# Kernel optimization log

Measured on AMD Instinct MI355X. Metric: run time of the kernel, lower is better.

Reference implementation:

```python
import jax, jax.numpy as jnp
import numpy as np

N = 20000      # nodes
E = 320000     # edges
F_IN = 64      # input_dim
HID = 128      # hidden_dim
H = 2          # heads (hard-coded in BGA)
G = 64         # num graphs (batch_step_dim[0])
MID = 32       # middle_dim
OUT = 1        # output_dim
EPS = 1e-5


def setup_inputs() -> dict:
    key = jax.random.key(0)
    ks = jax.random.split(key, 24)
    p = lambda k, shape: jax.random.normal(k, shape, jnp.float32) * 0.05
    inp = {}
    inp["x"] = jax.random.normal(ks[0], (N, F_IN), jnp.float32)
    inp["edge_index"] = jax.random.randint(ks[1], (2, E), 0, N)
    inp["atten_edge_index"] = jax.random.randint(ks[2], (2, E), 0, N)
    inp["batch_index"] = jnp.sort(jax.random.randint(ks[3], (N,), 0, G))
    # GANConv 0 MLP (2-layer: Linear->BN->ReLU->Linear)
    inp["g0_w1"] = p(ks[4], (F_IN, HID)); inp["g0_b1"] = jnp.zeros((HID,), jnp.float32)
    inp["g0_bn_g"] = jnp.ones((HID,), jnp.float32); inp["g0_bn_b"] = jnp.zeros((HID,), jnp.float32)
    inp["g0_w2"] = p(ks[5], (HID, HID)); inp["g0_b2"] = jnp.zeros((HID,), jnp.float32)
    # GANConv 1 MLP
    inp["g1_w1"] = p(ks[6], (HID, HID)); inp["g1_b1"] = jnp.zeros((HID,), jnp.float32)
    inp["g1_bn_g"] = jnp.ones((HID,), jnp.float32); inp["g1_bn_b"] = jnp.zeros((HID,), jnp.float32)
    inp["g1_w2"] = p(ks[7], (HID, HID)); inp["g1_b2"] = jnp.zeros((HID,), jnp.float32)
    # BGA batch norms after each GANConv
    inp["bn0_g"] = jnp.ones((HID,), jnp.float32); inp["bn0_b"] = jnp.zeros((HID,), jnp.float32)
    inp["bn1_g"] = jnp.ones((HID,), jnp.float32); inp["bn1_b"] = jnp.zeros((HID,), jnp.float32)
    # ATTConv atten_self: in=HID, out=HID, heads=2, concat=True
    inp["a1_wl"] = p(ks[8], (HID, H * HID)); inp["a1_bl"] = jnp.zeros((H * HID,), jnp.float32)
    inp["a1_wr"] = p(ks[9], (HID, H * HID)); inp["a1_br"] = jnp.zeros((H * HID,), jnp.float32)
    inp["a1_att"] = p(ks[10], (H, HID))
    inp["a1_bias"] = jnp.zeros((H * HID,), jnp.float32)
    # ATTConv atten: in=H*HID, out=HID, heads=2, concat=False (mean over heads)
    inp["a2_wl"] = p(ks[11], (H * HID, H * HID)); inp["a2_bl"] = jnp.zeros((H * HID,), jnp.float32)
    inp["a2_wr"] = p(ks[12], (H * HID, H * HID)); inp["a2_br"] = jnp.zeros((H * HID,), jnp.float32)
    inp["a2_att"] = p(ks[13], (H, HID))
    inp["a2_bias"] = jnp.zeros((HID,), jnp.float32)
    # prediction heads (only layer 0 and last are used)
    inp["pred0_w"] = p(ks[14], (F_IN, MID)); inp["pred0_b"] = jnp.zeros((MID,), jnp.float32)
    inp["predL_w"] = p(ks[15], (HID, MID)); inp["predL_b"] = jnp.zeros((MID,), jnp.float32)
    inp["out_w"] = p(ks[16], (MID, OUT)); inp["out_b"] = jnp.zeros((OUT,), jnp.float32)
    return inp


def _bn(x, g, b):  # training-mode batch norm over node axis
    m = x.mean(0)
    v = x.var(0)
    return (x - m) * jax.lax.rsqrt(v + EPS) * g + b


def _mlp2(x, w1, b1, bn_g, bn_b, w2, b2):
    h = jax.nn.relu(_bn(x @ w1 + b1, bn_g, bn_b))
    return h @ w2 + b2


def _gan_conv(x, edge_index, w1, b1, bn_g, bn_b, w2, b2):
    row, col = edge_index[0], edge_index[1]
    agg = jax.ops.segment_sum(x[col], row, num_segments=x.shape[0])
    return _mlp2(x + agg, w1, b1, bn_g, bn_b, w2, b2)


def _att_conv(x, edge_index, wl, bl, wr, br, att, bias, concat):
    # GATv2-style: e = leaky_relu(x_i + x_j); alpha = softmax_dst(<e, att>)
    n = x.shape[0]
    xl = (x @ wl + bl).reshape(n, H, HID)  # source proj
    xr = (x @ wr + br).reshape(n, H, HID)  # target proj
    src, dst = edge_index[0], edge_index[1]
    e = jax.nn.leaky_relu(xl[src] + xr[dst], 0.2)          # [E,H,C]
    logit = jnp.einsum('ehc,hc->eh', e, att)               # [E,H]
    lmax = jax.ops.segment_max(logit, dst, num_segments=n)
    w = jnp.exp(logit - lmax[dst])
    denom = jax.ops.segment_sum(w, dst, num_segments=n)
    alpha = w / (denom[dst] + 1e-16)                       # [E,H]
    out = jax.ops.segment_sum(xl[src] * alpha[:, :, None], dst, num_segments=n)
    if concat:
        out = out.reshape(n, H * HID)
    else:
        out = out.mean(1)
    return out + bias, alpha


def reference(x, edge_index, atten_edge_index, batch_index,
              g0_w1, g0_b1, g0_bn_g, g0_bn_b, g0_w2, g0_b2,
              g1_w1, g1_b1, g1_bn_g, g1_bn_b, g1_w2, g1_b2,
              bn0_g, bn0_b, bn1_g, bn1_b,
              a1_wl, a1_bl, a1_wr, a1_br, a1_att, a1_bias,
              a2_wl, a2_bl, a2_wr, a2_br, a2_att, a2_bias,
              pred0_w, pred0_b, predL_w, predL_b, out_w, out_b):
    h0 = x
    h1 = jax.nn.relu(_bn(_gan_conv(h0, edge_index, g0_w1, g0_b1, g0_bn_g, g0_bn_b, g0_w2, g0_b2), bn0_g, bn0_b))
    h2 = jax.nn.relu(_bn(_gan_conv(h1, edge_index, g1_w1, g1_b1, g1_bn_g, g1_bn_b, g1_w2, g1_b2), bn1_g, bn1_b))
    emb, _ = _att_conv(h2, edge_index, a1_wl, a1_bl, a1_wr, a1_br, a1_att, a1_bias, concat=True)
    emb = jax.nn.relu(emb)
    atten_out, alpha = _att_conv(emb, atten_edge_index, a2_wl, a2_bl, a2_wr, a2_br, a2_att, a2_bias, concat=False)
    atten_out = jax.nn.relu(atten_out)
    pool0 = jax.ops.segment_sum(h0, batch_index, num_segments=G)
    poolL = jax.ops.segment_sum(atten_out, batch_index, num_segments=G)
    out_h = jax.nn.relu((pool0 @ pred0_w + pred0_b) + (poolL @ predL_w + predL_b))
    outputs = out_h @ out_w + out_b
    return (outputs, atten_out, alpha)
```

## Files before the change

kernel.cpp:

```cpp
#include <hip/hip_runtime.h>
#include <hip/hip_bf16.h>

#define N_NODES 20000
#define E_EDGES 320000
#define F_INN   64
#define HID     128
#define HEADS   2
#define HC      (HEADS * HID)
#define G_GR    64
#define MIDD    32
#define EPSV    1e-5f
#define NBUK    79

#define CDIV(a, b) (((a) + (b) - 1) / (b))

typedef __attribute__((ext_vector_type(8))) short          bf16x8;
typedef __attribute__((ext_vector_type(4))) float          f32x4;
typedef __attribute__((ext_vector_type(8))) unsigned short u16x8;

__device__ inline float bf2f(unsigned short u) { return __uint_as_float((unsigned)u << 16); }
__device__ inline unsigned short f2bf(float f) {
    unsigned u = __float_as_uint(f);
    unsigned r = u + 0x7FFFu + ((u >> 16) & 1u);
    return (unsigned short)(r >> 16);
}

struct Csr3 {
    const int* key[3];
    const int* other[3];
    int* deg;
    int* rowptr[3];
    int* out[3];
    int2* tmp;
    int* bcur;
};

__global__ void k_hist3(Csr3 c) {
    int e = blockIdx.x * blockDim.x + threadIdx.x;
    int y = blockIdx.y;
    if (e < E_EDGES) atomicAdd(&c.deg[y * N_NODES + c.key[y][e]], 1);
}

__global__ __launch_bounds__(1024) void k_scan3(Csr3 c) {
    const int PER = (N_NODES + 1023) / 1024;
    __shared__ int part[1024];
    const int y = blockIdx.x;
    const int* deg = c.deg + y * N_NODES;
    int* rowptr = c.rowptr[y];
    const int tid = threadIdx.x;
    const int base = tid * PER;
    int lv[PER];
    int lsum = 0;
#pragma unroll
    for (int i = 0; i < PER; i++) {
        int idx = base + i;
        int v = (idx < N_NODES) ? deg[idx] : 0;
        lv[i] = v; lsum += v;
    }
    part[tid] = lsum;
    __syncthreads();
    for (int off = 1; off < 1024; off <<= 1) {
        int t = (tid >= off) ? part[tid - off] : 0;
        __syncthreads();
        part[tid] += t;
        __syncthreads();
    }
    int run = part[tid] - lsum;
    if (tid == 0) rowptr[0] = 0;
#pragma unroll
    for (int i = 0; i < PER; i++) {
        int idx = base + i;
        if (idx < N_NODES) {
            run += lv[i];
            rowptr[idx + 1] = run;
        }
        if (idx < N_NODES && i == 0) rowptr[idx] = part[tid] - lsum;
    }
    __syncthreads();
    if (tid < NBUK) c.bcur[y * NBUK + tid] = rowptr[tid << 8];
}

__global__ __launch_bounds__(256) void k_bucketA(Csr3 c) {
    __shared__ int hist[NBUK], base[NBUK], off[NBUK];
    const int y = blockIdx.y;
    const int chunk0 = blockIdx.x * 4096;
    const int t = threadIdx.x;
    for (int i = t; i < NBUK; i += 256) { hist[i] = 0; off[i] = 0; }
    __syncthreads();
    int keys[16], vals[16], bks[16];
#pragma unroll
    for (int i = 0; i < 16; i++) {
        int e = chunk0 + (i << 8) + t;
        bool ok = (e < E_EDGES);
        int k = ok ? c.key[y][e] : 0;
        keys[i] = k;
        vals[i] = ok ? ((y == 2) ? e : c.other[y][e]) : 0;
        bks[i] = ok ? (k >> 8) : -1;
        if (ok) atomicAdd(&hist[k >> 8], 1);
    }
    __syncthreads();
    if (t < NBUK && hist[t] > 0) base[t] = atomicAdd(&c.bcur[y * NBUK + t], hist[t]);
    __syncthreads();
    int2* ty = c.tmp + (size_t)y * E_EDGES;
#pragma unroll
    for (int i = 0; i < 16; i++) {
        int b = bks[i];
        if (b >= 0) {
            int o = atomicAdd(&off[b], 1);
            ty[base[b] + o] = make_int2(keys[i], vals[i]);
        }
    }
}

__global__ __launch_bounds__(256) void k_bucketB(Csr3 c) {
    __shared__ int cnt[256], lbase[256], run[256];
    const int y = blockIdx.y;
    const int b = blockIdx.x;
    const int nbase = b << 8;
    const int t = threadIdx.x;
    cnt[t] = 0; run[t] = 0;
    __syncthreads();
    const int* rowptr = c.rowptr[y];
    const int start = rowptr[nbase];
    const int nend = min(nbase + 256, N_NODES);
    const int end = rowptr[nend];
    const int2* ty = c.tmp + (size_t)y * E_EDGES;
    for (int i = start + t; i < end; i += 256)
        atomicAdd(&cnt[ty[i].x - nbase], 1);
    __syncthreads();
    int v = cnt[t];
    lbase[t] = v;
    __syncthreads();
    for (int off = 1; off < 256; off <<= 1) {
        int u = (t >= off) ? lbase[t - off] : 0;
        __syncthreads();
        lbase[t] += u;
        __syncthreads();
    }
    int excl = lbase[t] - v;
    __syncthreads();
    lbase[t] = excl;
    __syncthreads();
    int* outy = c.out[y];
    for (int i = start + t; i < end; i += 256) {
        int2 kv = ty[i];
        int k = kv.x - nbase;
        int o = atomicAdd(&run[k], 1);
        outy[start + lbase[k] + o] = kv.y;
    }
}

__global__ __launch_bounds__(256) void k_gather_f32(const float4* __restrict__ x,
                                                    const int* __restrict__ rowptr,
                                                    const int* __restrict__ srcs,
                                                    unsigned short* __restrict__ z) {
    int gid = blockIdx.x * blockDim.x + threadIdx.x;
    int n = gid >> 4;
    if (n >= N_NODES) return;
    int q = gid & 15;
    float4 acc = x[((size_t)n << 4) + q];
    int p1 = rowptr[n + 1];
    for (int p = rowptr[n]; p < p1; p++) {
        float4 v = x[((size_t)srcs[p] << 4) + q];
        acc.x += v.x; acc.y += v.y; acc.z += v.z; acc.w += v.w;
    }
    ushort4 o;
    o.x = f2bf(acc.x); o.y = f2bf(acc.y); o.z = f2bf(acc.z); o.w = f2bf(acc.w);
    *(ushort4*)&z[((size_t)n << 6) + (q << 2)] = o;
}

__global__ __launch_bounds__(256) void k_gather_bn(const u16x8* __restrict__ raw,
                                                   const int* __restrict__ rowptr,
                                                   const int* __restrict__ srcs,
                                                   const float* __restrict__ bn_sums,
                                                   const float* __restrict__ g,
                                                   const float* __restrict__ b,
                                                   u16x8* __restrict__ z) {
    int gid = blockIdx.x * blockDim.x + threadIdx.x;
    int n = gid >> 4;
    if (n >= N_NODES) return;
    int q = gid & 15;
    float sc[8], sh[8];
#pragma unroll
    for (int i = 0; i < 8; i++) {
        int c = (q << 3) + i;
        float mean = bn_sums[c] / N_NODES;
        float istd = rsqrtf(bn_sums[HID + c] / N_NODES - mean * mean + EPSV);
        float s = istd * g[c];
        sc[i] = s;
        sh[i] = b[c] - mean * s;
    }
    u16x8 u0 = raw[((size_t)n << 4) + q];
    float acc[8];
#pragma unroll
    for (int i = 0; i < 8; i++) acc[i] = fmaxf(bf2f(u0[i]) * sc[i] + sh[i], 0.f);
    int p1 = rowptr[n + 1];
    for (int p = rowptr[n]; p < p1; p++) {
        u16x8 v = raw[((size_t)srcs[p] << 4) + q];
#pragma unroll
        for (int i = 0; i < 8; i++) acc[i] += fmaxf(bf2f(v[i]) * sc[i] + sh[i], 0.f);
    }
    u16x8 o;
#pragma unroll
    for (int i = 0; i < 8; i++) o[i] = f2bf(acc[i]);
    z[((size_t)n << 4) + q] = o;
}

struct WtJob  { const float* src; unsigned short* dst; int K; int N; };
struct WtJobs { WtJob j[8]; };
__global__ void k_wt_cast(WtJobs jobs) {
    WtJob jb = jobs.j[blockIdx.y];
    int total = jb.K * jb.N;
    for (int i = blockIdx.x * blockDim.x + threadIdx.x; i < total; i += gridDim.x * blockDim.x) {
        int nn = i / jb.K, kk = i - nn * jb.K;
        jb.dst[i] = f2bf(jb.src[(size_t)kk * jb.N + nn]);
    }
}

template <int STATS, int BNA, int TM, int BIAS2>
__global__ __launch_bounds__(256) void k_mfma_gemm(const unsigned short* __restrict__ A,
                                                   const unsigned short* __restrict__ Wt,
                                                   const float* __restrict__ biasL,
                                                   const float* __restrict__ biasR,
                                                   unsigned short* __restrict__ Cout,
                                                   int M, int K, int N,
                                                   float* __restrict__ stats_sums,
                                                   const float* __restrict__ bn_sums,
                                                   const float* __restrict__ bn_g,
                                                   const float* __restrict__ bn_b) {
    constexpr int BNF = (TM == 128) ? 4 : 2;
    __shared__ unsigned short As[TM][40];
    __shared__ unsigned short Bs[128][40];
    __shared__ float s_scale[BNA ? HID : 1], s_shift[BNA ? HID : 1];
    const int t = threadIdx.x;
    if (BNA) {
        if (t < HID) {
            float mean = bn_sums[t] / M;
            float istd = rsqrtf(bn_sums[HID + t] / M - mean * mean + EPSV);
            float s = istd * bn_g[t];
            s_scale[t] = s;
            s_shift[t] = bn_b[t] - mean * s;
        }
        __syncthreads();
    }
    const int wave = t >> 6, lane = t & 63;
    const int row0 = blockIdx.y * TM, col0 = blockIdx.x * 128;
    const int wm = (TM == 128) ? ((wave & 1) << 6) : 0;
    const int wn = (TM == 128) ? ((wave >> 1) << 6) : (wave << 5);
    const int lm = lane & 15, lk = (lane >> 4) << 3;
    constexpr int APASS = TM / 64;
    f32x4 acc[4][BNF] = {};
    for (int k0 = 0; k0 < K; k0 += 32) {
        u16x8 av[APASS], wv[2];
#pragma unroll
        for (int i = 0; i < APASS; i++) {
            int c = t + (i << 8);
            int r = c >> 2, ko = (c & 3) << 3;
            u16x8 zv = {};
            int gr = row0 + r;
            av[i] = (gr < M) ? *(const u16x8*)&A[(size_t)gr * K + k0 + ko] : zv;
            if (BNA) {
#pragma unroll
                for (int j = 0; j < 8; j++) {
                    int kc = k0 + ko + j;
                    float v = fmaxf(bf2f(av[i][j]) * s_scale[kc] + s_shift[kc], 0.f);
                    av[i][j] = f2bf(v);
                }
            }
        }
#pragma unroll
        for (int i = 0; i < 2; i++) {
            int c = t + (i << 8);
            int r = c >> 2, ko = (c & 3) << 3;
            wv[i] = *(const u16x8*)&Wt[(size_t)(col0 + r) * K + k0 + ko];
        }
        __syncthreads();
#pragma unroll
        for (int i = 0; i < APASS; i++) {
            int c = t + (i << 8);
            int r = c >> 2, ko = (c & 3) << 3;
            *(u16x8*)&As[r][ko] = av[i];
        }
#pragma unroll
        for (int i = 0; i < 2; i++) {
            int c = t + (i << 8);
            int r = c >> 2, ko = (c & 3) << 3;
            *(u16x8*)&Bs[r][ko] = wv[i];
        }
        __syncthreads();
        bf16x8 af[4], bfm[BNF];
#pragma unroll
        for (int i = 0; i < 4; i++) af[i]  = *(const bf16x8*)&As[wm + (i << 4) + lm][lk];
#pragma unroll
        for (int j = 0; j < BNF; j++) bfm[j] = *(const bf16x8*)&Bs[wn + (j << 4) + lm][lk];
#pragma unroll
        for (int i = 0; i < 4; i++)
#pragma unroll
            for (int j = 0; j < BNF; j++)
                acc[i][j] = __builtin_amdgcn_mfma_f32_16x16x32_bf16(af[i], bfm[j], acc[i][j], 0, 0, 0);
    }
    const int lr4 = (lane >> 4) << 2;
    float s1[BNF], s2[BNF];
#pragma unroll
    for (int j = 0; j < BNF; j++) { s1[j] = 0.f; s2[j] = 0.f; }
#pragma unroll
    for (int j = 0; j < BNF; j++) {
        int col = col0 + wn + (j << 4) + lm;
        float bv = BIAS2 ? ((col < 256) ? biasL[col] : biasR[col - 256]) : biasL[col];
#pragma unroll
        for (int i = 0; i < 4; i++) {
#pragma unroll
            for (int r = 0; r < 4; r++) {
                int row = row0 + wm + (i << 4) + lr4 + r;
                if (row < M) {
                    float v = acc[i][j][r] + bv;
                    Cout[(size_t)row * N + col] = f2bf(v);
                    if (STATS) { s1[j] += v; s2[j] += v * v; }
                }
            }
        }
    }
    if (STATS) {
#pragma unroll
        for (int j = 0; j < BNF; j++) {
            s1[j] += __shfl_xor(s1[j], 16, 64); s1[j] += __shfl_xor(s1[j], 32, 64);
            s2[j] += __shfl_xor(s2[j], 16, 64); s2[j] += __shfl_xor(s2[j], 32, 64);
        }
        if ((lane >> 4) == 0) {
#pragma unroll
            for (int j = 0; j < BNF; j++) {
                int col = col0 + wn + (j << 4) + lm;
                atomicAdd(&stats_sums[col], s1[j]);
                atomicAdd(&stats_sums[HID + col], s2[j]);
            }
        }
    }
}

#define ATT_CAP 192
template <int CONCAT, int WITH_ALPHA>
__global__ __launch_bounds__(256) void k_att_fused(const ushort4* __restrict__ Q,
                                                   const int* __restrict__ rowptr,
                                                   const int* __restrict__ plist,
                                                   const int* __restrict__ other,
                                                   const float* __restrict__ att,
                                                   const float* __restrict__ bias,
                                                   void* __restrict__ outp,
                                                   float* __restrict__ alpha_out) {
    __shared__ float s_lg[4][ATT_CAP][2];
    const int t = threadIdx.x;
    const int wave = t >> 6, l = t & 63;
    const int n = blockIdx.x * 4 + wave;
    const int h = l >> 5;
    ushort4 ur = Q[((size_t)n << 7) + 64 + l];
    float xr4[4] = {bf2f(ur.x), bf2f(ur.y), bf2f(ur.z), bf2f(ur.w)};
    const float* ap = &att[h * HID + ((l & 31) << 2)];
    float at4[4] = {ap[0], ap[1], ap[2], ap[3]};
    const int p0 = rowptr[n], p1 = rowptr[n + 1];

    float m = -INFINITY, ssum = 0.f;
    float acc[4] = {0.f, 0.f, 0.f, 0.f};

#define ATT_SRC(p) (WITH_ALPHA ? other[plist[p]] : plist[p])

#define ATT_LOGIT(uv, x4, tl) do { \
        x4[0] = bf2f(uv.x); x4[1] = bf2f(uv.y); x4[2] = bf2f(uv.z); x4[3] = bf2f(uv.w); \
        float v0 = x4[0] + xr4[0]; v0 = (v0 > 0.f) ? v0 : 0.2f * v0; \
        float v1 = x4[1] + xr4[1]; v1 = (v1 > 0.f) ? v1 : 0.2f * v1; \
        float v2 = x4[2] + xr4[2]; v2 = (v2 > 0.f) ? v2 : 0.2f * v2; \
        float v3 = x4[3] + xr4[3]; v3 = (v3 > 0.f) ? v3 : 0.2f * v3; \
        tl = at4[0] * v0 + at4[1] * v1 + at4[2] * v2 + at4[3] * v3; \
    } while (0)

#define ATT_ONLINE(x4, tl, idx) do { \
        float mn = fmaxf(m, tl); \
        float sc = __expf(m - mn); \
        float w  = __expf(tl - mn); \
        ssum = ssum * sc + w; \
        acc[0] = acc[0] * sc + w * x4[0]; \
        acc[1] = acc[1] * sc + w * x4[1]; \
        acc[2] = acc[2] * sc + w * x4[2]; \
        acc[3] = acc[3] * sc + w * x4[3]; \
        m = mn; \
        if (WITH_ALPHA && (idx) < ATT_CAP && (l & 31) == 0) s_lg[wave][idx][h] = tl; \
    } while (0)

    int p = p0;
    for (; p + 4 <= p1; p += 4) {
        float x4[4][4], tl[4];
        ushort4 uv[4];
        int ss[4];
#pragma unroll
        for (int j = 0; j < 4; j++) ss[j] = ATT_SRC(p + j);
#pragma unroll
        for (int j = 0; j < 4; j++) uv[j] = Q[((size_t)ss[j] << 7) + l];
#pragma unroll
        for (int j = 0; j < 4; j++) ATT_LOGIT(uv[j], x4[j], tl[j]);
#pragma unroll
        for (int k = 1; k <= 16; k <<= 1) {
#pragma unroll
            for (int j = 0; j < 4; j++) tl[j] += __shfl_xor(tl[j], k, 64);
        }
#pragma unroll
        for (int j = 0; j < 4; j++) ATT_ONLINE(x4[j], tl[j], p + j - p0);
    }
    for (; p < p1; p++) {
        float x4[4], tl;
        ushort4 uv = Q[((size_t)ATT_SRC(p) << 7) + l];
        ATT_LOGIT(uv, x4, tl);
#pragma unroll
        for (int k = 1; k <= 16; k <<= 1) tl += __shfl_xor(tl, k, 64);
        ATT_ONLINE(x4, tl, p - p0);
    }
    float inv = 1.f / (ssum + 1e-16f);

    if (WITH_ALPHA) {
        float m_o   = __shfl_xor(m, 32, 64);
        float inv_o = __shfl_xor(inv, 32, 64);
        float m2[2], i2[2];
        m2[h] = m; m2[1 - h] = m_o;
        i2[h] = inv; i2[1 - h] = inv_o;
        int cnt = p1 - p0;
        int ccnt = (cnt < ATT_CAP) ? cnt : ATT_CAP;
        for (int i = l; i < ccnt * 2; i += 64) {
            int idx = i >> 1, hh = i & 1;
            float a = __expf(s_lg[wave][idx][hh] - m2[hh]) * i2[hh];
            alpha_out[plist[p0 + idx] * HEADS + hh] = a;
        }
        for (int pp = p0 + ATT_CAP; pp < p1; pp++) {
            float x4[4], tl;
            ushort4 uv = Q[((size_t)ATT_SRC(pp) << 7) + l];
            ATT_LOGIT(uv, x4, tl);
#pragma unroll
            for (int k = 1; k <= 16; k <<= 1) tl += __shfl_xor(tl, k, 64);
            if ((l & 31) == 0) alpha_out[plist[pp] * HEADS + h] = __expf(tl - m) * inv;
        }
    }

    if (CONCAT) {
        const float* bp = &bias[l << 2];
        ushort4 o;
        o.x = f2bf(fmaxf(acc[0] * inv + bp[0], 0.f));
        o.y = f2bf(fmaxf(acc[1] * inv + bp[1], 0.f));
        o.z = f2bf(fmaxf(acc[2] * inv + bp[2], 0.f));
        o.w = f2bf(fmaxf(acc[3] * inv + bp[3], 0.f));
        ((ushort4*)outp)[((size_t)n << 6) + l] = o;
    } else {
        float o[4];
#pragma unroll
        for (int i = 0; i < 4; i++) {
            float v = acc[i] * inv;
            float other_v = __shfl_xor(v, 32, 64);
            o[i] = 0.5f * (v + other_v);
        }
        if (l < 32) {
            const float* bp = &bias[(l & 31) << 2];
            float4 ov;
            ov.x = fmaxf(o[0] + bp[0], 0.f); ov.y = fmaxf(o[1] + bp[1], 0.f);
            ov.z = fmaxf(o[2] + bp[2], 0.f); ov.w = fmaxf(o[3] + bp[3], 0.f);
            ((float4*)outp)[((size_t)n << 5) + l] = ov;
        }
    }
#undef ATT_SRC
#undef ATT_LOGIT
#undef ATT_ONLINE
}

template <int C>
__global__ __launch_bounds__(256) void k_pool_atomic(const float* __restrict__ X,
                                                     const int* __restrict__ batch,
                                                     float* __restrict__ pool, int npb) {
    const int RP = 256 / C;
    int c = threadIdx.x & (C - 1);
    int rofs = threadIdx.x / C;
    int i0 = blockIdx.x * npb;
    int i1 = min(i0 + npb, N_NODES);
    float acc = 0.f;
    int gcur = -1;
    for (int i = i0 + rofs; i < i1; i += RP) {
        int g = batch[i];
        if (g != gcur) {
            if (gcur >= 0) atomicAdd(&pool[gcur * C + c], acc);
            acc = 0.f; gcur = g;
        }
        acc += X[(size_t)i * C + c];
    }
    if (gcur >= 0) atomicAdd(&pool[gcur * C + c], acc);
}

__global__ void k_head(const float* __restrict__ pool0, const float* __restrict__ poolL,
                       const float* __restrict__ p0w, const float* __restrict__ p0b,
                       const float* __restrict__ pLw, const float* __restrict__ pLb,
                       const float* __restrict__ ow, const float* __restrict__ ob,
                       float* __restrict__ outputs) {
    int g = blockIdx.x;
    int m = threadIdx.x;
    __shared__ float sh[MIDD];
    if (m < MIDD) {
        float s = p0b[m] + pLb[m];
        for (int k = 0; k < F_INN; k++) s += pool0[g * F_INN + k] * p0w[k * MIDD + m];
        for (int k = 0; k < HID; k++)  s += poolL[g * HID + k] * pLw[k * MIDD + m];
        sh[m] = fmaxf(s, 0.f);
    }
    __syncthreads();
    if (m == 0) {
        float s = ob[0];
        for (int k = 0; k < MIDD; k++) s += sh[k] * ow[k];
        outputs[g] = s;
    }
}

extern "C" void kernel_launch(void* const* d_in, const int* in_sizes, int n_in,
                              void* d_out, int out_size, void* d_ws, size_t ws_size,
                              hipStream_t stream) {
    const float* x      = (const float*)d_in[0];
    const int*   ei     = (const int*)d_in[1];
    const int*   aei    = (const int*)d_in[2];
    const int*   batch  = (const int*)d_in[3];
    const float* g0_w1  = (const float*)d_in[4];
    const float* g0_b1  = (const float*)d_in[5];
    const float* g0_bng = (const float*)d_in[6];
    const float* g0_bnb = (const float*)d_in[7];
    const float* g0_w2  = (const float*)d_in[8];
    const float* g0_b2  = (const float*)d_in[9];
    const float* g1_w1  = (const float*)d_in[10];
    const float* g1_b1  = (const float*)d_in[11];
    const float* g1_bng = (const float*)d_in[12];
    const float* g1_bnb = (const float*)d_in[13];
    const float* g1_w2  = (const float*)d_in[14];
    const float* g1_b2  = (const float*)d_in[15];
    const float* bn0_g  = (const float*)d_in[16];
    const float* bn0_b  = (const float*)d_in[17];
    const float* bn1_g  = (const float*)d_in[18];
    const float* bn1_b  = (const float*)d_in[19];
    const float* a1_wl  = (const float*)d_in[20];
    const float* a1_bl  = (const float*)d_in[21];
    const float* a1_wr  = (const float*)d_in[22];
    const float* a1_br  = (const float*)d_in[23];
    const float* a1_att = (const float*)d_in[24];
    const float* a1_bias= (const float*)d_in[25];
    const float* a2_wl  = (const float*)d_in[26];
    const float* a2_bl  = (const float*)d_in[27];
    const float* a2_wr  = (const float*)d_in[28];
    const float* a2_br  = (const float*)d_in[29];
    const float* a2_att = (const float*)d_in[30];
    const float* a2_bias= (const float*)d_in[31];
    const float* p0w    = (const float*)d_in[32];
    const float* p0b    = (const float*)d_in[33];
    const float* pLw    = (const float*)d_in[34];
    const float* pLb    = (const float*)d_in[35];
    const float* ow     = (const float*)d_in[36];
    const float* ob     = (const float*)d_in[37];

    float* out_head  = (float*)d_out;
    float* atten_out = out_head + G_GR;
    float* alpha_out = atten_out + (size_t)N_NODES * HID;

    float* ws = (float*)d_ws;
    float* sums4 = ws;
    float* pool0 = sums4 + 4 * 256;
    float* poolL = pool0 + G_GR * F_INN;
    int*   deg3  = (int*)(poolL + G_GR * HID);
    const size_t zero_bytes = (4 * 256 + G_GR * F_INN + G_GR * HID + 3 * N_NODES) * 4;

    int* ip = deg3 + 3 * N_NODES;
    int* bcur = ip; ip += 3 * NBUK;
    int* rowptr[3]; int* payload[3];
    for (int c = 0; c < 3; c++) {
        rowptr[c]  = ip; ip += N_NODES + 1;
        payload[c] = ip; ip += E_EDGES;
    }
    int2* tmp3 = (int2*)ip; ip += 2 * 3 * E_EDGES;
    const size_t NB = (size_t)N_NODES * HC;
    unsigned short* B1 = (unsigned short*)ip;
    unsigned short* B2 = B1 + NB;
    unsigned short* Qb = B2 + NB;
    unsigned short* g0w1t = Qb + 2 * NB;
    unsigned short* g0w2t = g0w1t + 128 * 64;
    unsigned short* g1w1t = g0w2t + 128 * 128;
    unsigned short* g1w2t = g1w1t + 128 * 128;
    unsigned short* a1wlt = g1w2t + 128 * 128;
    unsigned short* a1wrt = a1wlt + 256 * 128;
    unsigned short* a2wlt = a1wrt + 256 * 128;
    unsigned short* a2wrt = a2wlt + 256 * 256;

    const int* e_row = ei;
    const int* e_col = ei + E_EDGES;
    const int* a_src = aei;
    const int* a_dst = aei + E_EDGES;

    const int TB = 256;
#define GRID1(n) dim3(CDIV((n), TB))

    {
        WtJobs jobs;
        jobs.j[0] = {g0_w1, g0w1t, F_INN, HID};
        jobs.j[1] = {g0_w2, g0w2t, HID,   HID};
        jobs.j[2] = {g1_w1, g1w1t, HID,   HID};
        jobs.j[3] = {g1_w2, g1w2t, HID,   HID};
        jobs.j[4] = {a1_wl, a1wlt, HID,   HC};
        jobs.j[5] = {a1_wr, a1wrt, HID,   HC};
        jobs.j[6] = {a2_wl, a2wlt, HC,    HC};
        jobs.j[7] = {a2_wr, a2wrt, HC,    HC};
        k_wt_cast<<<dim3(32, 8), TB, 0, stream>>>(jobs);
    }

    hipMemsetAsync(sums4, 0, zero_bytes, stream);
    {
        Csr3 c;
        c.key[0] = e_row; c.other[0] = e_col;
        c.key[1] = e_col; c.other[1] = e_row;
        c.key[2] = a_dst; c.other[2] = a_src;
        c.deg = deg3; c.tmp = tmp3; c.bcur = bcur;
        for (int i = 0; i < 3; i++) { c.rowptr[i] = rowptr[i]; c.out[i] = payload[i]; }
        k_hist3<<<dim3(CDIV(E_EDGES, TB), 3), TB, 0, stream>>>(c);
        k_scan3<<<dim3(3), 1024, 0, stream>>>(c);
        k_bucketA<<<dim3(CDIV(E_EDGES, 4096), 3), TB, 0, stream>>>(c);
        k_bucketB<<<dim3(NBUK, 3), TB, 0, stream>>>(c);
    }

    const dim3 gemm_g1(1, CDIV(N_NODES, 64));
    const dim3 gemm_gq(4, CDIV(N_NODES, 128));
    const float* NOF = nullptr;

    k_gather_f32<<<GRID1(N_NODES * 16), TB, 0, stream>>>((const float4*)x, rowptr[0], payload[0], B1);
    k_mfma_gemm<1, 0, 64, 0><<<gemm_g1, TB, 0, stream>>>(B1, g0w1t, g0_b1, NOF, B2, N_NODES, F_INN, HID,
                                                         sums4 + 0, NOF, NOF, NOF);
    k_mfma_gemm<1, 1, 64, 0><<<gemm_g1, TB, 0, stream>>>(B2, g0w2t, g0_b2, NOF, B1, N_NODES, HID, HID,
                                                         sums4 + 256, sums4 + 0, g0_bng, g0_bnb);

    k_gather_bn<<<GRID1(N_NODES * 16), TB, 0, stream>>>((const u16x8*)B1, rowptr[0], payload[0],
                                                        sums4 + 256, bn0_g, bn0_b, (u16x8*)B2);
    k_mfma_gemm<1, 0, 64, 0><<<gemm_g1, TB, 0, stream>>>(B2, g1w1t, g1_b1, NOF, B1, N_NODES, HID, HID,
                                                         sums4 + 512, NOF, NOF, NOF);
    k_mfma_gemm<1, 1, 64, 0><<<gemm_g1, TB, 0, stream>>>(B1, g1w2t, g1_b2, NOF, B2, N_NODES, HID, HID,
                                                         sums4 + 768, sums4 + 512, g1_bng, g1_bnb);

    k_mfma_gemm<0, 1, 128, 1><<<gemm_gq, TB, 0, stream>>>(B2, a1wlt, a1_bl, a1_br, Qb, N_NODES, HID, 512,
                                                          nullptr, sums4 + 768, bn1_g, bn1_b);
    k_att_fused<1, 0><<<dim3(N_NODES / 4), TB, 0, stream>>>(
        (const ushort4*)Qb, rowptr[1], payload[1], nullptr, a1_att, a1_bias, (void*)B1, nullptr);

    k_mfma_gemm<0, 0, 128, 1><<<gemm_gq, TB, 0, stream>>>(B1, a2wlt, a2_bl, a2_br, Qb, N_NODES, HC, 512,
                                                          nullptr, NOF, NOF, NOF);
    k_att_fused<0, 1><<<dim3(N_NODES / 4), TB, 0, stream>>>(
        (const ushort4*)Qb, rowptr[2], payload[2], a_src, a2_att, a2_bias, (void*)atten_out, alpha_out);

    {
        const int npb = 64;
        k_pool_atomic<F_INN><<<dim3(CDIV(N_NODES, npb)), TB, 0, stream>>>(x, batch, pool0, npb);
        k_pool_atomic<HID><<<dim3(CDIV(N_NODES, npb)), TB, 0, stream>>>(atten_out, batch, poolL, npb);
    }
    k_head<<<dim3(G_GR), 64, 0, stream>>>(pool0, poolL, p0w, p0b, pLw, pLb, ow, ob, out_head);
}
```

Before: 484.7 us.

## Build CSR via bucket-level histogram and batch online-softmax updates per four edges

Replaces the per-node global-atomic degree histogram and 20000-entry scan with a shared-memory histogram over 79 coarse buckets, a tiny bucket scan, and row pointers computed inside the second bucket pass. This cuts global atomics and the serial 1024-thread scan from the CSR build. Separately, the attention loop now does one online-softmax rescale per four edges using their combined max instead of four sequential rescales, storing logits for alpha inline. The batched update changes the floating-point rounding order slightly.

```diff
diff --git a/kernel.cpp b/kernel.cpp
--- a/kernel.cpp
+++ b/kernel.cpp
@@ -28,56 +28,46 @@
 struct Csr3 {
     const int* key[3];
     const int* other[3];
-    int* deg;
+    int* btot;
+    int* bstart;
+    int* bcur;
     int* rowptr[3];
     int* out[3];
     int2* tmp;
-    int* bcur;
 };
 
-__global__ void k_hist3(Csr3 c) {
-    int e = blockIdx.x * blockDim.x + threadIdx.x;
-    int y = blockIdx.y;
-    if (e < E_EDGES) atomicAdd(&c.deg[y * N_NODES + c.key[y][e]], 1);
-}
-
-__global__ __launch_bounds__(1024) void k_scan3(Csr3 c) {
-    const int PER = (N_NODES + 1023) / 1024;
-    __shared__ int part[1024];
-    const int y = blockIdx.x;
-    const int* deg = c.deg + y * N_NODES;
-    int* rowptr = c.rowptr[y];
-    const int tid = threadIdx.x;
-    const int base = tid * PER;
-    int lv[PER];
-    int lsum = 0;
-#pragma unroll
-    for (int i = 0; i < PER; i++) {
-        int idx = base + i;
-        int v = (idx < N_NODES) ? deg[idx] : 0;
-        lv[i] = v; lsum += v;
-    }
-    part[tid] = lsum;
-    __syncthreads();
-    for (int off = 1; off < 1024; off <<= 1) {
-        int t = (tid >= off) ? part[tid - off] : 0;
-        __syncthreads();
-        part[tid] += t;
-        __syncthreads();
-    }
-    int run = part[tid] - lsum;
-    if (tid == 0) rowptr[0] = 0;
-#pragma unroll
-    for (int i = 0; i < PER; i++) {
-        int idx = base + i;
-        if (idx < N_NODES) {
-            run += lv[i];
-            rowptr[idx + 1] = run;
-        }
-        if (idx < N_NODES && i == 0) rowptr[idx] = part[tid] - lsum;
-    }
-    __syncthreads();
-    if (tid < NBUK) c.bcur[y * NBUK + tid] = rowptr[tid << 8];
+__global__ __launch_bounds__(256) void k_bhist(Csr3 c) {
+    __shared__ int hist[NBUK];
+    const int y = blockIdx.y;
+    const int chunk0 = blockIdx.x * 4096;
+    const int t = threadIdx.x;
+    for (int i = t; i < NBUK; i += 256) hist[i] = 0;
+    __syncthreads();
+#pragma unroll
+    for (int i = 0; i < 16; i++) {
+        int e = chunk0 + (i << 8) + t;
+        if (e < E_EDGES) atomicAdd(&hist[c.key[y][e] >> 8], 1);
+    }
+    __syncthreads();
+    for (int i = t; i < NBUK; i += 256)
+        if (hist[i] > 0) atomicAdd(&c.btot[y * NBUK + i], hist[i]);
+}
+
+__global__ void k_bscan(Csr3 c) {
+    __shared__ int sh[3 * NBUK];
+    int t = threadIdx.x;
+    for (int i = t; i < 3 * NBUK; i += 256) sh[i] = c.btot[i];
+    __syncthreads();
+    if (t < 3) {
+        int run = 0;
+        int* bs = c.bstart + t * (NBUK + 1);
+        for (int b = 0; b < NBUK; b++) {
+            bs[b] = run;
+            c.bcur[t * NBUK + b] = run;
+            run += sh[t * NBUK + b];
+        }
+        bs[NBUK] = run;
+    }
 }
 
 __global__ __launch_bounds__(256) void k_bucketA(Csr3 c) {
@@ -120,12 +110,10 @@
     const int t = threadIdx.x;
     cnt[t] = 0; run[t] = 0;
     __syncthreads();
-    const int* rowptr = c.rowptr[y];
-    const int start = rowptr[nbase];
-    const int nend = min(nbase + 256, N_NODES);
-    const int end = rowptr[nend];
+    const int bs = c.bstart[y * (NBUK + 1) + b];
+    const int be = c.bstart[y * (NBUK + 1) + b + 1];
     const int2* ty = c.tmp + (size_t)y * E_EDGES;
-    for (int i = start + t; i < end; i += 256)
+    for (int i = bs + t; i < be; i += 256)
         atomicAdd(&cnt[ty[i].x - nbase], 1);
     __syncthreads();
     int v = cnt[t];
@@ -141,12 +129,15 @@
     __syncthreads();
     lbase[t] = excl;
     __syncthreads();
+    int n = nbase + t;
+    if (n < N_NODES) c.rowptr[y][n] = bs + excl;
+    if (b == NBUK - 1 && t == 0) c.rowptr[y][N_NODES] = E_EDGES;
     int* outy = c.out[y];
-    for (int i = start + t; i < end; i += 256) {
+    for (int i = bs + t; i < be; i += 256) {
         int2 kv = ty[i];
         int k = kv.x - nbase;
         int o = atomicAdd(&run[k], 1);
-        outy[start + lbase[k] + o] = kv.y;
+        outy[bs + lbase[k] + o] = kv.y;
     }
 }
 
@@ -401,8 +392,21 @@
 #pragma unroll
             for (int j = 0; j < 4; j++) tl[j] += __shfl_xor(tl[j], k, 64);
         }
-#pragma unroll
-        for (int j = 0; j < 4; j++) ATT_ONLINE(x4[j], tl[j], p + j - p0);
+        if (WITH_ALPHA && (l & 31) == 0) {
+#pragma unroll
+            for (int j = 0; j < 4; j++)
+                if (p + j - p0 < ATT_CAP) s_lg[wave][p + j - p0][h] = tl[j];
+        }
+        float tmax = fmaxf(fmaxf(tl[0], tl[1]), fmaxf(tl[2], tl[3]));
+        float mn = fmaxf(m, tmax);
+        float sc = __expf(m - mn);
+        float w0 = __expf(tl[0] - mn), w1 = __expf(tl[1] - mn);
+        float w2 = __expf(tl[2] - mn), w3 = __expf(tl[3] - mn);
+        ssum = ssum * sc + (w0 + w1 + w2 + w3);
+#pragma unroll
+        for (int c = 0; c < 4; c++)
+            acc[c] = acc[c] * sc + w0 * x4[0][c] + w1 * x4[1][c] + w2 * x4[2][c] + w3 * x4[3][c];
+        m = mn;
     }
     for (; p < p1; p++) {
         float x4[4], tl;
@@ -560,11 +564,12 @@
     float* sums4 = ws;
     float* pool0 = sums4 + 4 * 256;
     float* poolL = pool0 + G_GR * F_INN;
-    int*   deg3  = (int*)(poolL + G_GR * HID);
-    const size_t zero_bytes = (4 * 256 + G_GR * F_INN + G_GR * HID + 3 * N_NODES) * 4;
-
-    int* ip = deg3 + 3 * N_NODES;
-    int* bcur = ip; ip += 3 * NBUK;
+    int*   btot  = (int*)(poolL + G_GR * HID);
+    const size_t zero_bytes = (4 * 256 + G_GR * F_INN + G_GR * HID + 3 * NBUK) * 4;
+
+    int* ip = btot + 3 * NBUK;
+    int* bstart = ip; ip += 3 * (NBUK + 1);
+    int* bcur   = ip; ip += 3 * NBUK;
     int* rowptr[3]; int* payload[3];
     for (int c = 0; c < 3; c++) {
         rowptr[c]  = ip; ip += N_NODES + 1;
@@ -611,10 +616,10 @@
         c.key[0] = e_row; c.other[0] = e_col;
         c.key[1] = e_col; c.other[1] = e_row;
         c.key[2] = a_dst; c.other[2] = a_src;
-        c.deg = deg3; c.tmp = tmp3; c.bcur = bcur;
+        c.btot = btot; c.bstart = bstart; c.bcur = bcur; c.tmp = tmp3;
         for (int i = 0; i < 3; i++) { c.rowptr[i] = rowptr[i]; c.out[i] = payload[i]; }
-        k_hist3<<<dim3(CDIV(E_EDGES, TB), 3), TB, 0, stream>>>(c);
-        k_scan3<<<dim3(3), 1024, 0, stream>>>(c);
+        k_bhist<<<dim3(CDIV(E_EDGES, 4096), 3), TB, 0, stream>>>(c);
+        k_bscan<<<dim3(1), TB, 0, stream>>>(c);
         k_bucketA<<<dim3(CDIV(E_EDGES, 4096), 3), TB, 0, stream>>>(c);
         k_bucketB<<<dim3(NBUK, 3), TB, 0, stream>>>(c);
     }
```

After: 446.0 us. -8.0%, faster.
